# Optimization experiments

Hardware: AMD Instinct MI355X
Metric: run time of the kernel (lower is better)

The kernel has to match this reference:

```python
import jax, jax.numpy as jnp
import numpy as np

COST_CLASS, COST_BBOX, COST_GIOU = 1.0, 5.0, 2.0


def box_cxcywh_to_xyxy(b):
    cx, cy, w, h = jnp.split(b, 4, axis=-1)
    return jnp.concatenate([cx - 0.5 * w, cy - 0.5 * h, cx + 0.5 * w, cy + 0.5 * h], axis=-1)


def generalized_box_iou(a, b):
    # a: [N,4], b: [T,4] in xyxy -> [N,T]
    area_a = (a[:, 2] - a[:, 0]) * (a[:, 3] - a[:, 1])
    area_b = (b[:, 2] - b[:, 0]) * (b[:, 3] - b[:, 1])
    lt = jnp.maximum(a[:, None, :2], b[None, :, :2])
    rb = jnp.minimum(a[:, None, 2:], b[None, :, 2:])
    wh = jnp.clip(rb - lt, 0.0)
    inter = wh[..., 0] * wh[..., 1]
    union = area_a[:, None] + area_b[None, :] - inter
    iou = inter / union
    lt_e = jnp.minimum(a[:, None, :2], b[None, :, :2])
    rb_e = jnp.maximum(a[:, None, 2:], b[None, :, 2:])
    wh_e = jnp.clip(rb_e - lt_e, 0.0)
    area_e = wh_e[..., 0] * wh_e[..., 1]
    return iou - (area_e - union) / area_e


def cost_matrix(pred_logits, pred_boxes, tgt_labels, tgt_boxes):
    B, Q, _ = pred_logits.shape
    probs = jax.nn.softmax(pred_logits.reshape(B * Q, -1), axis=-1)
    pb = pred_boxes.reshape(B * Q, 4)
    tl = tgt_labels.reshape(-1)
    tb = tgt_boxes.reshape(-1, 4)
    cc = -probs[:, tl]                                              # [BQ, BM]
    cb = jnp.sum(jnp.abs(pb[:, None, :] - tb[None, :, :]), axis=-1)  # L1 cdist
    cg = -generalized_box_iou(box_cxcywh_to_xyxy(pb), box_cxcywh_to_xyxy(tb))
    C = COST_CLASS * cc + COST_BBOX * cb + COST_GIOU * cg
    return C.reshape(B, Q, -1)


def hungarian(cost):
    # Jonker-Volgenant shortest-augmenting-path assignment.
    # cost: [n, m] with n <= m; returns the column assigned to each row, [n] int32.
    n, m = cost.shape
    INF = jnp.float32(1e30)

    def solve_row(i, uvp):
        u, v, p = uvp  # u:[n+1] row potentials (+dummy), v:[m+1], p:[m+1] row assigned per col
        p = p.at[m].set(i)  # virtual start column m holds the new row
        state = (jnp.int32(m), u, v, p,
                 jnp.full(m + 1, INF, jnp.float32),   # minv
                 jnp.zeros(m + 1, bool),              # used
                 jnp.zeros(m + 1, jnp.int32))         # way

        def cond(s):
            j0, _, _, p, _, _, _ = s
            return p[j0] != -1

        def body(s):
            j0, u, v, p, minv, used, way = s
            used = used.at[j0].set(True)
            i0 = p[j0]
            cur = jnp.where(used[:m], INF, cost[i0] - u[i0] - v[:m])
            better = cur < minv[:m]
            minv = minv.at[:m].set(jnp.where(better, cur, minv[:m]))
            way = way.at[:m].set(jnp.where(better, j0, way[:m]))
            masked = jnp.where(used[:m], INF, minv[:m])
            j1 = jnp.argmin(masked).astype(jnp.int32)
            delta = masked[j1]
            u = u.at[jnp.where(used, p, n)].add(jnp.where(used, delta, 0.0))
            v = jnp.where(used, v - delta, v)
            minv = jnp.where(used, minv, minv - delta)
            return (j1, u, v, p, minv, used, way)

        j0, u, v, p, minv, used, way = jax.lax.while_loop(cond, body, state)

        def a_cond(s):
            return s[0] != m

        def a_body(s):
            j0, p = s
            j1 = way[j0]
            return (j1, p.at[j0].set(p[j1]))

        _, p = jax.lax.while_loop(a_cond, a_body, (j0, p))
        return (u, v, p)

    u0 = jnp.zeros(n + 1, jnp.float32)
    v0 = jnp.zeros(m + 1, jnp.float32)
    p0 = jnp.full(m + 1, -1, jnp.int32)
    _, _, p = jax.lax.fori_loop(0, n, solve_row, (u0, v0, p0))
    row_of_col = p[:m]
    cols = jnp.arange(m, dtype=jnp.int32)
    col_of_row = jnp.zeros(n + 1, jnp.int32).at[
        jnp.where(row_of_col >= 0, row_of_col, n)].set(cols)
    return col_of_row[:n]


def setup_inputs() -> dict:
    key = jax.random.key(0)
    k1, k2, k3, k4 = jax.random.split(key, 4)
    B, Q, NCLS, M = 32, 300, 92, 50
    return {
        'pred_logits': jax.random.normal(k1, (B, Q, NCLS), jnp.float32),
        'pred_boxes': jax.random.uniform(k2, (B, Q, 4), dtype=jnp.float32),
        'tgt_labels': jax.random.randint(k3, (B, M), 0, NCLS),
        'tgt_boxes': jax.random.uniform(k4, (B, M, 4), dtype=jnp.float32),
    }


def reference(pred_logits, pred_boxes, tgt_labels, tgt_boxes):
    B, Q, _ = pred_logits.shape
    M = tgt_labels.shape[1]
    C = cost_matrix(pred_logits, pred_boxes, tgt_labels, tgt_boxes)  # [B, Q, B*M]
    # per-image block of columns: C[i, :, i*M:(i+1)*M]
    C4 = C.reshape(B, Q, B, M)
    C_per = jnp.transpose(jnp.diagonal(C4, axis1=0, axis2=2), (2, 0, 1))  # [B, Q, M]
    q = jax.vmap(hungarian)(jnp.transpose(C_per, (0, 2, 1)))  # [B, M]: query per target
    order = jnp.argsort(q, axis=1).astype(jnp.int32)
    pred_idx = jnp.take_along_axis(q, order, axis=1)  # sorted query indices
    gt_idx = order                                     # matching target indices
    return pred_idx, gt_idx, C
```

## Files before the change

kernel.cpp:

```cpp
#include <hip/hip_runtime.h>

#define NB   32
#define NQ   300
#define NCLS 92
#define NM   50
#define BM   (NB * NM)
#define BQ   (NB * NQ)
#define HM   NQ
#define HN   NM
#define PITCH 305
#define BIG  1e30f
#define HUNG_BLOCKS NB
#define COST_ROWS_PER_BLOCK 16
#define COST_BLOCKS (BQ / COST_ROWS_PER_BLOCK)
#define NBLOCKS (HUNG_BLOCKS + COST_BLOCKS)

typedef float vf4 __attribute__((ext_vector_type(4)));

#define FENCE() __threadfence_block()

#define DPP_XOR1  0xB1
#define DPP_XOR2  0x4E
#define DPP_HMIRR 0x141
#define DPP_MIRR  0x140
#define DPP_BC15  0x142
#define DPP_BC31  0x143

template <int C_>
__device__ __forceinline__ float dppk(float v) {
  return __int_as_float(__builtin_amdgcn_update_dpp(
      __float_as_int(v), __float_as_int(v), C_, 0xf, 0xf, false));
}
template <int C_>
__device__ __forceinline__ float dppz(float v) {
  return __int_as_float(
      __builtin_amdgcn_update_dpp(0, __float_as_int(v), C_, 0xf, 0xf, true));
}

__device__ __forceinline__ float rl63(float v) {
  return __int_as_float(__builtin_amdgcn_readlane(__float_as_int(v), 63));
}
__device__ __forceinline__ int rli(int v, int l) {
  return __builtin_amdgcn_readlane(v, l);
}
__device__ __forceinline__ float rlf(float v, int l) {
  return __int_as_float(__builtin_amdgcn_readlane(__float_as_int(v), l));
}
__device__ __forceinline__ float frcp(float x) {
  return __builtin_amdgcn_rcpf(x);
}

__device__ __forceinline__ float wredu_max(float v) {
  v = fmaxf(v, dppk<DPP_XOR1>(v));
  v = fmaxf(v, dppk<DPP_XOR2>(v));
  v = fmaxf(v, dppk<DPP_HMIRR>(v));
  v = fmaxf(v, dppk<DPP_MIRR>(v));
  v = fmaxf(v, dppk<DPP_BC15>(v));
  v = fmaxf(v, dppk<DPP_BC31>(v));
  return rl63(v);
}
__device__ __forceinline__ float wredu_min(float v) {
  v = fminf(v, dppk<DPP_XOR1>(v));
  v = fminf(v, dppk<DPP_XOR2>(v));
  v = fminf(v, dppk<DPP_HMIRR>(v));
  v = fminf(v, dppk<DPP_MIRR>(v));
  v = fminf(v, dppk<DPP_BC15>(v));
  v = fminf(v, dppk<DPP_BC31>(v));
  return rl63(v);
}
__device__ __forceinline__ float wredu_sum(float v) {
  v += dppz<DPP_XOR1>(v);
  v += dppz<DPP_XOR2>(v);
  v += dppz<DPP_HMIRR>(v);
  v += dppz<DPP_MIRR>(v);
  v += dppz<DPP_BC15>(v);
  v += dppz<DPP_BC31>(v);
  return rl63(v);
}

#define RLSEL(dst, kk, ll, a0, a1, a2, a3, a4)        \
  {                                                   \
    if ((kk) == 0)      dst = rli((a0), (ll));        \
    else if ((kk) == 1) dst = rli((a1), (ll));        \
    else if ((kk) == 2) dst = rli((a2), (ll));        \
    else if ((kk) == 3) dst = rli((a3), (ll));        \
    else                dst = rli((a4), (ll));        \
  }
#define WRSEL(kk, ll, val, a0, a1, a2, a3, a4)        \
  {                                                   \
    if (lane == (ll)) {                               \
      if ((kk) == 0)      a0 = (val);                 \
      else if ((kk) == 1) a1 = (val);                 \
      else if ((kk) == 2) a2 = (val);                 \
      else if ((kk) == 3) a3 = (val);                 \
      else                a4 = (val);                 \
    }                                                 \
  }

__device__ __forceinline__ float pair_cost(float ax1, float ay1, float ax2,
                                           float ay2, float areaA,
                                           const float4& pb, const float4& t,
                                           float negprob) {
  float cb = fabsf(pb.x - t.x) + fabsf(pb.y - t.y) +
             fabsf(pb.z - t.z) + fabsf(pb.w - t.w);
  float bx1 = t.x - 0.5f * t.z, by1 = t.y - 0.5f * t.w;
  float bx2 = t.x + 0.5f * t.z, by2 = t.y + 0.5f * t.w;
  float areaB = (bx2 - bx1) * (by2 - by1);
  float iw = fmaxf(fminf(ax2, bx2) - fmaxf(ax1, bx1), 0.f);
  float ih = fmaxf(fminf(ay2, by2) - fmaxf(ay1, by1), 0.f);
  float inter = iw * ih;
  float uni = areaA + areaB - inter;
  float iou = inter * frcp(uni);
  float ew = fmaxf(fmaxf(ax2, bx2) - fminf(ax1, bx1), 0.f);
  float eh = fmaxf(fmaxf(ay2, by2) - fminf(ay1, by1), 0.f);
  float areaE = ew * eh;
  float giou = iou - (areaE - uni) * frcp(areaE);
  return (negprob + 5.f * cb) - 2.f * giou;
}

__device__ __forceinline__ void wave_softmax(const float* __restrict__ lrow,
                                             float* prow, int lane) {
  float x0 = lrow[lane];
  float x1 = (lane + 64 < NCLS) ? lrow[lane + 64] : -BIG;
  float mx = wredu_max(fmaxf(x0, x1));
  float e0 = expf(x0 - mx), e1 = expf(x1 - mx);
  float s = wredu_sum(e0 + e1);
  float rs = frcp(s);
  prow[lane] = e0 * rs;
  if (lane + 64 < NCLS) prow[lane + 64] = e1 * rs;
}

__global__ __launch_bounds__(1024, 8) void fused_kernel(
    const float* __restrict__ logits, const float* __restrict__ pboxes,
    const int* __restrict__ tlab, const float* __restrict__ tbox,
    float* __restrict__ outp) {
  __shared__ float hc[HN * PITCH];
  __shared__ float probs_s[16][NCLS];
  __shared__ int   qarr[HN];

  float* C = outp + 2 * BM;
  int tid = threadIdx.x, wave = tid >> 6, lane = tid & 63;

  if (blockIdx.x >= HUNG_BLOCKS) {
    int row = (blockIdx.x - HUNG_BLOCKS) * COST_ROWS_PER_BLOCK + wave;
    wave_softmax(logits + (size_t)row * NCLS, probs_s[wave], lane);

    float4 pb = reinterpret_cast<const float4*>(pboxes)[row];
    float ax1 = pb.x - 0.5f * pb.z, ay1 = pb.y - 0.5f * pb.w;
    float ax2 = pb.x + 0.5f * pb.z, ay2 = pb.y + 0.5f * pb.w;
    float areaA = (ax2 - ax1) * (ay2 - ay1);

    const float4* tbv = reinterpret_cast<const float4*>(tbox);
    const int4*   tlv = reinterpret_cast<const int4*>(tlab);
    vf4* crow = reinterpret_cast<vf4*>(C + (size_t)row * BM);
#pragma unroll 2
    for (int q4 = lane; q4 < BM / 4; q4 += 64) {
      int4 cls = tlv[q4];
      int clsa[4] = {cls.x, cls.y, cls.z, cls.w};
      vf4 o;
#pragma unroll
      for (int e = 0; e < 4; e++) {
        float4 t = tbv[q4 * 4 + e];
        o[e] = pair_cost(ax1, ay1, ax2, ay2, areaA, pb, t,
                         -probs_s[wave][clsa[e]]);
      }
      __builtin_nontemporal_store(o, &crow[q4]);
    }
    return;
  }

  int b = blockIdx.x;

  float4 t_reg = make_float4(0.f, 0.f, 0.f, 0.f);
  int cls_reg = 0;
  if (lane < NM) {
    t_reg = reinterpret_cast<const float4*>(tbox)[b * NM + lane];
    cls_reg = tlab[b * NM + lane];
  }

  const float4* pbv = reinterpret_cast<const float4*>(pboxes);
#pragma unroll 2
  for (int q = wave; q < NQ; q += 16) {
    const float* lrow = logits + (size_t)(b * NQ + q) * NCLS;
    float x0 = lrow[lane];
    float x1 = (lane + 64 < NCLS) ? lrow[lane + 64] : -BIG;
    float mx = wredu_max(fmaxf(x0, x1));
    float e0 = expf(x0 - mx), e1 = expf(x1 - mx);
    float s = wredu_sum(e0 + e1);
    float g0 = __shfl(x0, cls_reg, 64);
    float g1 = __shfl(x1, cls_reg, 64);
    float xsel = (cls_reg < 64) ? g0 : g1;
    float negp = -(expf(xsel - mx) * frcp(s));

    float4 pb = pbv[b * NQ + q];
    float ax1 = pb.x - 0.5f * pb.z, ay1 = pb.y - 0.5f * pb.w;
    float ax2 = pb.x + 0.5f * pb.z, ay2 = pb.y + 0.5f * pb.w;
    float areaA = (ax2 - ax1) * (ay2 - ay1);
    if (lane < NM) {
      hc[lane * PITCH + q] =
          pair_cost(ax1, ay1, ax2, ay2, areaA, pb, t_reg, negp);
    }
  }
  __syncthreads();
  if (wave != 0) return;

  __builtin_amdgcn_s_setprio(1);


  float u_reg = 0.f;
  int am_reg = 0;
  if (lane < HN) {
    const float* r = &hc[lane * PITCH];
    float mn0 = BIG, mn1 = BIG;
    int a0 = 0, a1 = 1;
    for (int j = 0; j < HM; j += 2) {
      float va = r[j], vb = r[j + 1];
      if (va < mn0) { mn0 = va; a0 = j; }
      if (vb < mn1) { mn1 = vb; a1 = j + 1; }
    }
    bool takeOdd = (mn1 < mn0) || (mn1 == mn0 && a1 < a0);
    u_reg = takeOdd ? mn1 : mn0;
    am_reg = takeOdd ? a1 : a0;
  }

  int pr0 = -1, pr1 = -1, pr2 = -1, pr3 = -1, pr4 = -1;
  int wy0 = 0, wy1 = 0, wy2 = 0, wy3 = 0, wy4 = 0;

  unsigned amask = 0;
  unsigned long long pending = 0;
  for (int i = 0; i < HN; i++) {
    int jm = rli(am_reg, i);
    unsigned mrem = (unsigned)rli((int)amask, jm & 63);
    if (!((mrem >> (jm >> 6)) & 1u)) {
      if (lane == (jm & 63)) amask |= 1u << (jm >> 6);
      int kk = jm >> 6, ll = jm & 63;
      WRSEL(kk, ll, i, pr0, pr1, pr2, pr3, pr4);
    } else {
      pending |= 1ull << i;
    }
  }

  float v_r[5], minv_r[5], h[5];
#pragma unroll
  for (int k = 0; k < 5; k++) v_r[k] = 0.f;

  while (pending) {
    int i_start = (int)__ffsll((long long)pending) - 1;
    pending &= pending - 1;
#pragma unroll
    for (int k = 0; k < 5; k++) minv_r[k] = BIG;
    unsigned usedc = 0;
    unsigned long long used_rows = 1ull << i_start;
    int i0 = i_start, j0 = HM, jfree = -1;
    float ui0 = rlf(u_reg, i0);

#pragma unroll
    for (int k = 0; k < 5; k++) {
      int j = lane + 64 * k;
      h[k] = (j < HM) ? hc[i0 * PITCH + j] : BIG;
    }

    while (true) {
      float bk[5];
#pragma unroll
      for (int k = 0; k < 5; k++) {
        int j = lane + 64 * k;
        bool act = (j < HM) && !((usedc >> k) & 1u);
        float cur = h[k] - ui0 - v_r[k];
        if (act && cur < minv_r[k]) {
          minv_r[k] = cur;
          if (k == 0) wy0 = j0; else if (k == 1) wy1 = j0;
          else if (k == 2) wy2 = j0; else if (k == 3) wy3 = j0;
          else wy4 = j0;
        }
        bk[k] = act ? minv_r[k] : BIG;
      }
      float m01 = (bk[1] < bk[0]) ? bk[1] : bk[0];
      int   j01 = (bk[1] < bk[0]) ? lane + 64 : lane;
      float m23 = (bk[3] < bk[2]) ? bk[3] : bk[2];
      int   j23 = (bk[3] < bk[2]) ? lane + 192 : lane + 128;
      float m03 = (m23 < m01) ? m23 : m01;
      int   j03 = (m23 < m01) ? j23 : j01;
      float best = (bk[4] < m03) ? bk[4] : m03;
      int   bj   = (bk[4] < m03) ? lane + 256 : j03;

      float wmin = wredu_min(best);
      unsigned long long ball = __ballot(best == wmin);
      int src = (int)__ffsll((long long)ball) - 1;
      int j1 = rli(bj, src);
      float delta = wmin;

      int psel;
      {
        int kk = j1 >> 6, ll = j1 & 63;
        RLSEL(psel, kk, ll, pr0, pr1, pr2, pr3, pr4);
      }

      if (psel != -1) {
#pragma unroll
        for (int k = 0; k < 5; k++) {
          int j = lane + 64 * k;
          h[k] = (j < HM) ? hc[psel * PITCH + j] : BIG;
        }
      }

      if ((used_rows >> lane) & 1ull) u_reg += delta;
#pragma unroll
      for (int k = 0; k < 5; k++) {
        int j = lane + 64 * k;
        if (j < HM) {
          if ((usedc >> k) & 1u) v_r[k] -= delta;
          else                   minv_r[k] -= delta;
        }
      }
      if (lane == (j1 & 63)) usedc |= 1u << (j1 >> 6);

      if (psel == -1) { jfree = j1; break; }
      i0 = psel;
      used_rows |= 1ull << i0;
      ui0 = rlf(u_reg, i0);
      j0 = j1;
    }

    int jj = jfree;
    while (jj != HM) {
      int kk = jj >> 6, ll = jj & 63;
      int jn;
      RLSEL(jn, kk, ll, wy0, wy1, wy2, wy3, wy4);
      int pv;
      if (jn == HM) {
        pv = i_start;
      } else {
        int k2 = jn >> 6, l2 = jn & 63;
        RLSEL(pv, k2, l2, pr0, pr1, pr2, pr3, pr4);
      }
      WRSEL(kk, ll, pv, pr0, pr1, pr2, pr3, pr4);
      jj = jn;
    }
  }

  {
    int j, r;
    j = lane;       r = pr0; if (r >= 0) qarr[r] = j;
    j = lane + 64;  r = pr1; if (r >= 0) qarr[r] = j;
    j = lane + 128; r = pr2; if (r >= 0) qarr[r] = j;
    j = lane + 192; r = pr3; if (r >= 0) qarr[r] = j;
    j = lane + 256; r = pr4; if (j < HM && r >= 0) qarr[r] = j;
  }
  FENCE();
  if (lane < HN) {
    int qi = qarr[lane];
    int rank = 0;
    for (int t = 0; t < HN; t++) rank += (qarr[t] < qi);
    outp[(size_t)b * NM + rank] = (float)qi;
    outp[BM + (size_t)b * NM + rank] = (float)lane;
  }
}

extern "C" void kernel_launch(void* const* d_in, const int* in_sizes, int n_in,
                              void* d_out, int out_size, void* d_ws, size_t ws_size,
                              hipStream_t stream) {
  const float* logits = (const float*)d_in[0];
  const float* pboxes = (const float*)d_in[1];
  const int*   tlab   = (const int*)d_in[2];
  const float* tbox   = (const float*)d_in[3];
  float* out = (float*)d_out;

  fused_kernel<<<dim3(NBLOCKS), dim3(1024), 0, stream>>>(
      logits, pboxes, tlab, tbox, out);
}
```

Before: 122.1 us.

## Pack row assignments into bitfields, fuse row-min into cost build, prefetch logits

The five per-slot row-assignment registers are packed into one 30-bit word of 6-bit fields, so a lookup becomes a single lane read plus a shift instead of a branchy select. Each wave now tracks a per-target running min and argmin while it fills the cost tile, and wave 0 reduces these 16 partials instead of rescanning 300 columns. The cost-build loop software-prefetches the next query's logits and box, and wave priorities are raised. Inner-loop updates become branchless selects, and the next row's cost is always reloaded to avoid divergence, at the price of a redundant shared-memory load.

```diff
diff --git a/kernel.cpp b/kernel.cpp
--- a/kernel.cpp
+++ b/kernel.cpp
@@ -77,25 +77,6 @@
   v += dppz<DPP_BC31>(v);
   return rl63(v);
 }
-
-#define RLSEL(dst, kk, ll, a0, a1, a2, a3, a4)        \
-  {                                                   \
-    if ((kk) == 0)      dst = rli((a0), (ll));        \
-    else if ((kk) == 1) dst = rli((a1), (ll));        \
-    else if ((kk) == 2) dst = rli((a2), (ll));        \
-    else if ((kk) == 3) dst = rli((a3), (ll));        \
-    else                dst = rli((a4), (ll));        \
-  }
-#define WRSEL(kk, ll, val, a0, a1, a2, a3, a4)        \
-  {                                                   \
-    if (lane == (ll)) {                               \
-      if ((kk) == 0)      a0 = (val);                 \
-      else if ((kk) == 1) a1 = (val);                 \
-      else if ((kk) == 2) a2 = (val);                 \
-      else if ((kk) == 3) a3 = (val);                 \
-      else                a4 = (val);                 \
-    }                                                 \
-  }
 
 __device__ __forceinline__ float pair_cost(float ax1, float ay1, float ax2,
                                            float ay2, float areaA,
@@ -137,6 +118,8 @@
   __shared__ float hc[HN * PITCH];
   __shared__ float probs_s[16][NCLS];
   __shared__ int   qarr[HN];
+  __shared__ float pmn_s[16][64];
+  __shared__ int   pam_s[16][64];
 
   float* C = outp + 2 * BM;
   int tid = threadIdx.x, wave = tid >> 6, lane = tid & 63;
@@ -170,6 +153,7 @@
   }
 
   int b = blockIdx.x;
+  __builtin_amdgcn_s_setprio(1);
 
   float4 t_reg = make_float4(0.f, 0.f, 0.f, 0.f);
   int cls_reg = 0;
@@ -179,62 +163,75 @@
   }
 
   const float4* pbv = reinterpret_cast<const float4*>(pboxes);
-#pragma unroll 2
-  for (int q = wave; q < NQ; q += 16) {
+  float pmn = BIG;
+  int pam = 0;
+  {
+    int q = wave;
     const float* lrow = logits + (size_t)(b * NQ + q) * NCLS;
     float x0 = lrow[lane];
     float x1 = (lane + 64 < NCLS) ? lrow[lane + 64] : -BIG;
-    float mx = wredu_max(fmaxf(x0, x1));
-    float e0 = expf(x0 - mx), e1 = expf(x1 - mx);
-    float s = wredu_sum(e0 + e1);
-    float g0 = __shfl(x0, cls_reg, 64);
-    float g1 = __shfl(x1, cls_reg, 64);
-    float xsel = (cls_reg < 64) ? g0 : g1;
-    float negp = -(expf(xsel - mx) * frcp(s));
-
-    float4 pb = pbv[b * NQ + q];
-    float ax1 = pb.x - 0.5f * pb.z, ay1 = pb.y - 0.5f * pb.w;
-    float ax2 = pb.x + 0.5f * pb.z, ay2 = pb.y + 0.5f * pb.w;
-    float areaA = (ax2 - ax1) * (ay2 - ay1);
-    if (lane < NM) {
-      hc[lane * PITCH + q] =
-          pair_cost(ax1, ay1, ax2, ay2, areaA, pb, t_reg, negp);
-    }
-  }
+    float4 pbq = pbv[b * NQ + q];
+    while (q < NQ) {
+      int qn = q + 16;
+      int qc = (qn < NQ) ? qn : q;
+      const float* lrn = logits + (size_t)(b * NQ + qc) * NCLS;
+      float nx0 = lrn[lane];
+      float nx1 = (lane + 64 < NCLS) ? lrn[lane + 64] : -BIG;
+      float4 npb = pbv[b * NQ + qc];
+
+      float mx = wredu_max(fmaxf(x0, x1));
+      float e0 = expf(x0 - mx), e1 = expf(x1 - mx);
+      float s = wredu_sum(e0 + e1);
+      float g0 = __shfl(x0, cls_reg, 64);
+      float g1 = __shfl(x1, cls_reg, 64);
+      float xsel = (cls_reg < 64) ? g0 : g1;
+      float negp = -(expf(xsel - mx) * frcp(s));
+
+      float ax1 = pbq.x - 0.5f * pbq.z, ay1 = pbq.y - 0.5f * pbq.w;
+      float ax2 = pbq.x + 0.5f * pbq.z, ay2 = pbq.y + 0.5f * pbq.w;
+      float areaA = (ax2 - ax1) * (ay2 - ay1);
+      if (lane < NM) {
+        float cc = pair_cost(ax1, ay1, ax2, ay2, areaA, pbq, t_reg, negp);
+        hc[lane * PITCH + q] = cc;
+        if (cc < pmn) { pmn = cc; pam = q; }
+      }
+      x0 = nx0; x1 = nx1; pbq = npb; q = qn;
+    }
+  }
+  pmn_s[wave][lane] = pmn;
+  pam_s[wave][lane] = pam;
   __syncthreads();
   if (wave != 0) return;
 
-  __builtin_amdgcn_s_setprio(1);
-
+  __builtin_amdgcn_s_setprio(3);
 
   float u_reg = 0.f;
   int am_reg = 0;
   if (lane < HN) {
-    const float* r = &hc[lane * PITCH];
-    float mn0 = BIG, mn1 = BIG;
-    int a0 = 0, a1 = 1;
-    for (int j = 0; j < HM; j += 2) {
-      float va = r[j], vb = r[j + 1];
-      if (va < mn0) { mn0 = va; a0 = j; }
-      if (vb < mn1) { mn1 = vb; a1 = j + 1; }
-    }
-    bool takeOdd = (mn1 < mn0) || (mn1 == mn0 && a1 < a0);
-    u_reg = takeOdd ? mn1 : mn0;
-    am_reg = takeOdd ? a1 : a0;
-  }
-
-  int pr0 = -1, pr1 = -1, pr2 = -1, pr3 = -1, pr4 = -1;
+    float mn = pmn_s[0][lane];
+    int am = pam_s[0][lane];
+#pragma unroll
+    for (int w = 1; w < 16; w++) {
+      float v = pmn_s[w][lane];
+      int a = pam_s[w][lane];
+      bool t = (v < mn) || (v == mn && a < am);
+      mn = t ? v : mn;
+      am = t ? a : am;
+    }
+    u_reg = mn;
+    am_reg = am;
+  }
+
+  int pr_pk = 0x3FFFFFFF;
   int wy0 = 0, wy1 = 0, wy2 = 0, wy3 = 0, wy4 = 0;
 
-  unsigned amask = 0;
   unsigned long long pending = 0;
   for (int i = 0; i < HN; i++) {
     int jm = rli(am_reg, i);
-    unsigned mrem = (unsigned)rli((int)amask, jm & 63);
-    if (!((mrem >> (jm >> 6)) & 1u)) {
-      if (lane == (jm & 63)) amask |= 1u << (jm >> 6);
-      int kk = jm >> 6, ll = jm & 63;
-      WRSEL(kk, ll, i, pr0, pr1, pr2, pr3, pr4);
+    int kk = jm >> 6, ll = jm & 63, sh = kk * 6;
+    int word = rli(pr_pk, ll);
+    if (((word >> sh) & 63) == 63) {
+      if (lane == ll) pr_pk = (pr_pk & ~(63 << sh)) | (i << sh);
     } else {
       pending |= 1ull << i;
     }
@@ -254,26 +251,29 @@
     int i0 = i_start, j0 = HM, jfree = -1;
     float ui0 = rlf(u_reg, i0);
 
-#pragma unroll
-    for (int k = 0; k < 5; k++) {
-      int j = lane + 64 * k;
-      h[k] = (j < HM) ? hc[i0 * PITCH + j] : BIG;
+    {
+      int ro = i0 * PITCH;
+      h[0] = hc[ro + lane];
+      h[1] = hc[ro + lane + 64];
+      h[2] = hc[ro + lane + 128];
+      h[3] = hc[ro + lane + 192];
+      h[4] = (lane < 44) ? hc[ro + lane + 256] : BIG;
     }
 
     while (true) {
       float bk[5];
 #pragma unroll
       for (int k = 0; k < 5; k++) {
-        int j = lane + 64 * k;
-        bool act = (j < HM) && !((usedc >> k) & 1u);
+        bool uk = (usedc >> k) & 1u;
         float cur = h[k] - ui0 - v_r[k];
-        if (act && cur < minv_r[k]) {
-          minv_r[k] = cur;
-          if (k == 0) wy0 = j0; else if (k == 1) wy1 = j0;
-          else if (k == 2) wy2 = j0; else if (k == 3) wy3 = j0;
-          else wy4 = j0;
-        }
-        bk[k] = act ? minv_r[k] : BIG;
+        bool upd = !uk && (cur < minv_r[k]);
+        minv_r[k] = upd ? cur : minv_r[k];
+        if (k == 0) wy0 = upd ? j0 : wy0;
+        else if (k == 1) wy1 = upd ? j0 : wy1;
+        else if (k == 2) wy2 = upd ? j0 : wy2;
+        else if (k == 3) wy3 = upd ? j0 : wy3;
+        else wy4 = upd ? j0 : wy4;
+        bk[k] = uk ? BIG : minv_r[k];
       }
       float m01 = (bk[1] < bk[0]) ? bk[1] : bk[0];
       int   j01 = (bk[1] < bk[0]) ? lane + 64 : lane;
@@ -290,30 +290,29 @@
       int j1 = rli(bj, src);
       float delta = wmin;
 
-      int psel;
+      int ll = j1 & 63, kk = j1 >> 6, sh = kk * 6;
+      int word = rli(pr_pk, ll);
+      int praw = (word >> sh) & 63;
+      int psel = (praw == 63) ? -1 : praw;
+
       {
-        int kk = j1 >> 6, ll = j1 & 63;
-        RLSEL(psel, kk, ll, pr0, pr1, pr2, pr3, pr4);
-      }
-
-      if (psel != -1) {
-#pragma unroll
-        for (int k = 0; k < 5; k++) {
-          int j = lane + 64 * k;
-          h[k] = (j < HM) ? hc[psel * PITCH + j] : BIG;
-        }
-      }
-
-      if ((used_rows >> lane) & 1ull) u_reg += delta;
+        int pf = (psel < 0) ? i0 : psel;
+        int ro = pf * PITCH;
+        h[0] = hc[ro + lane];
+        h[1] = hc[ro + lane + 64];
+        h[2] = hc[ro + lane + 128];
+        h[3] = hc[ro + lane + 192];
+        h[4] = (lane < 44) ? hc[ro + lane + 256] : BIG;
+      }
+
+      u_reg += ((used_rows >> lane) & 1ull) ? delta : 0.f;
 #pragma unroll
       for (int k = 0; k < 5; k++) {
-        int j = lane + 64 * k;
-        if (j < HM) {
-          if ((usedc >> k) & 1u) v_r[k] -= delta;
-          else                   minv_r[k] -= delta;
-        }
-      }
-      if (lane == (j1 & 63)) usedc |= 1u << (j1 >> 6);
+        bool uk = (usedc >> k) & 1u;
+        v_r[k]    = uk ? v_r[k] - delta : v_r[k];
+        minv_r[k] = uk ? minv_r[k] : minv_r[k] - delta;
+      }
+      usedc |= ((lane == ll) ? 1u : 0u) << kk;
 
       if (psel == -1) { jfree = j1; break; }
       i0 = psel;
@@ -324,28 +323,31 @@
 
     int jj = jfree;
     while (jj != HM) {
-      int kk = jj >> 6, ll = jj & 63;
+      int kk = jj >> 6, ll = jj & 63, sh = kk * 6;
       int jn;
-      RLSEL(jn, kk, ll, wy0, wy1, wy2, wy3, wy4);
+      if (kk == 0) jn = rli(wy0, ll);
+      else if (kk == 1) jn = rli(wy1, ll);
+      else if (kk == 2) jn = rli(wy2, ll);
+      else if (kk == 3) jn = rli(wy3, ll);
+      else jn = rli(wy4, ll);
       int pv;
       if (jn == HM) {
         pv = i_start;
       } else {
         int k2 = jn >> 6, l2 = jn & 63;
-        RLSEL(pv, k2, l2, pr0, pr1, pr2, pr3, pr4);
-      }
-      WRSEL(kk, ll, pv, pr0, pr1, pr2, pr3, pr4);
+        int w2 = rli(pr_pk, l2);
+        pv = (w2 >> (k2 * 6)) & 63;
+      }
+      if (lane == ll) pr_pk = (pr_pk & ~(63 << sh)) | (pv << sh);
       jj = jn;
     }
   }
 
-  {
-    int j, r;
-    j = lane;       r = pr0; if (r >= 0) qarr[r] = j;
-    j = lane + 64;  r = pr1; if (r >= 0) qarr[r] = j;
-    j = lane + 128; r = pr2; if (r >= 0) qarr[r] = j;
-    j = lane + 192; r = pr3; if (r >= 0) qarr[r] = j;
-    j = lane + 256; r = pr4; if (j < HM && r >= 0) qarr[r] = j;
+#pragma unroll
+  for (int k = 0; k < 5; k++) {
+    int r = (pr_pk >> (k * 6)) & 63;
+    int j = lane + 64 * k;
+    if (r != 63) qarr[r] = j;
   }
   FENCE();
   if (lane < HN) {
```

Result: faster. 110.7 us (-9.3%).
